# Performance work log

Hardware: AMD Instinct MI355X
Metric: run time of the kernel (lower is better)

## Reference

```python
import jax, jax.numpy as jnp
import numpy as np

N, FIN, F, H = 4096, 128, 64, 8
NEG = -1e10


def setup_inputs() -> dict:
    key = jax.random.key(0)
    ks = jax.random.split(key, 6)
    X = jax.random.normal(ks[0], (N, FIN), dtype=jnp.float32)
    # sparse-ish binary adjacency with self loops, stored dense (as the layer expects)
    A = (jax.random.uniform(ks[1], (N, N)) < 0.05).astype(jnp.int32)
    A = A.at[jnp.arange(N), jnp.arange(N)].set(1)
    W = jax.random.normal(ks[2], (H, FIN, F), dtype=jnp.float32) * (1.0 / np.sqrt(FIN))
    b = jnp.zeros((H, F), dtype=jnp.float32)
    a_self = jax.random.normal(ks[3], (H, F), dtype=jnp.float32) * (1.0 / np.sqrt(F))
    a_neigh = jax.random.normal(ks[4], (H, F), dtype=jnp.float32) * (1.0 / np.sqrt(F))
    return {"X": X, "A": A, "W": W, "b": b, "a_self": a_self, "a_neigh": a_neigh}


def reference(X, A, W, b, a_self, a_neigh):
    # Dropout layers run in inference mode in the original call -> identity.
    feats = jnp.einsum('nf,hfo->hno', X, W)              # [H, N, F]
    s_self = jnp.einsum('hno,ho->hn', feats, a_self)     # [H, N]
    s_neigh = jnp.einsum('hno,ho->hn', feats, a_neigh)   # [H, N]
    scores = s_self[:, :, None] + s_neigh[:, None, :]    # [H, N, N]
    scores = jnp.where(scores > 0, scores, 0.2 * scores)  # LeakyReLU(0.2)
    mask = (1.0 - A.astype(jnp.float32)) * NEG            # [N, N]
    attn = jax.nn.softmax(scores + mask[None], axis=-1)   # [H, N, N]
    out = jnp.einsum('hnm,hmo->hno', attn, feats) + b[:, None, :]
    out = jax.nn.elu(out)                                 # [H, N, F]
    # concat heads -> [N, H*F]
    return jnp.transpose(out, (1, 0, 2)).reshape(N, H * F)
```

## Files before the change

### kernel.cpp

```cpp
#include <hip/hip_runtime.h>
#include <cmath>


#define NN 4096
#define FIN 128
#define FF 64
#define HH 8

typedef _Float16 h2 __attribute__((ext_vector_type(2)));
typedef _Float16 h4 __attribute__((ext_vector_type(4)));
typedef _Float16 h8 __attribute__((ext_vector_type(8)));
typedef float f32x2 __attribute__((ext_vector_type(2)));
typedef float f32x4 __attribute__((ext_vector_type(4)));

union H8 {
  h8 v;
  h2 p[4];
};
union H4 {
  h4 v;
  h2 p[2];
};

static __device__ __forceinline__ float dot2acc(h2 a, float c) {
#if __has_builtin(__builtin_amdgcn_fdot2)
  return __builtin_amdgcn_fdot2(a, (h2){(_Float16)1.f, (_Float16)1.f}, c,
                                false);
#else
  return c + (float)a[0] + (float)a[1];
#endif
}

static __device__ __forceinline__ void gload16(const void* g, void* l) {
  __builtin_amdgcn_global_load_lds(
      (const __attribute__((address_space(1))) unsigned int*)g,
      (__attribute__((address_space(3))) unsigned int*)l, 16, 0, 0);
}

static __device__ __forceinline__ void pack_row(const int* __restrict__ A,
                                                unsigned long long* __restrict__
                                                    bits,
                                                int row, int tid) {
  __shared__ int ldsT[4][4][256];
  const int wave = tid >> 6, lane = tid & 63;
  const int* ar = A + (size_t)row * NN;
  int4 v[4];
#pragma unroll
  for (int it = 0; it < 4; ++it) {
    const int g = wave * 4 + it;
    v[it] = *(const int4*)(ar + g * 256 + lane * 4);
  }
#pragma unroll
  for (int it = 0; it < 4; ++it) *(int4*)&ldsT[wave][it][lane * 4] = v[it];
  unsigned long long* br = bits + ((size_t)row << 6);
#pragma unroll
  for (int it = 0; it < 4; ++it) {
    const int g = wave * 4 + it;
    int w0 = ldsT[wave][it][0 * 64 + lane];
    int w1 = ldsT[wave][it][1 * 64 + lane];
    int w2 = ldsT[wave][it][2 * 64 + lane];
    int w3 = ldsT[wave][it][3 * 64 + lane];
    unsigned long long m0 = __ballot(w0 != 0);
    unsigned long long m1 = __ballot(w1 != 0);
    unsigned long long m2 = __ballot(w2 != 0);
    unsigned long long m3 = __ballot(w3 != 0);
    if (lane == 0) {
      ulonglong2 p0 = {m0, m1}, p1 = {m2, m3};
      *(ulonglong2*)(br + g * 4 + 0) = p0;
      *(ulonglong2*)(br + g * 4 + 2) = p1;
    }
  }
}

__global__ __launch_bounds__(256) void k1_kernel(
    const int* __restrict__ A, const float* __restrict__ W,
    const float* __restrict__ X, unsigned long long* __restrict__ bits,
    _Float16* __restrict__ Wsw, _Float16* __restrict__ Xsw) {
  const int b = blockIdx.x;
  const int tid = threadIdx.x;
  const int wave = tid >> 6, lane = tid & 63;
  if (b < 2) {
    const int h0 = b * 4;
    for (int h = h0; h < h0 + 4; ++h) {
      for (int c = tid; c < 1024; c += 256) {
        int ln = c & 63, nb = (c >> 6) & 3, kt = c >> 8;
        int f = nb * 16 + (ln & 15);
        int k0 = kt * 32 + (ln >> 4) * 8;
        h8 v;
#pragma unroll
        for (int j = 0; j < 8; ++j)
          v[j] = (_Float16)W[((size_t)(h * FIN) + k0 + j) * FF + f];
        *(h8*)(Wsw + ((size_t)(((h * 4 + kt) * 4 + nb) * 64 + ln)) * 8) = v;
      }
    }
  } else if (b < 66) {
    const int tile = (b - 2) * 4 + wave;
    const int l16 = lane & 15, quad = lane >> 4;
    const float* xr = X + (size_t)(tile * 16 + l16) * FIN;
#pragma unroll
    for (int kt = 0; kt < 4; ++kt) {
      int k0 = kt * 32 + quad * 8;
      f32x4 x0 = *(const f32x4*)(xr + k0);
      f32x4 x1 = *(const f32x4*)(xr + k0 + 4);
      h8 v = {(_Float16)x0[0], (_Float16)x0[1], (_Float16)x0[2],
              (_Float16)x0[3], (_Float16)x1[0], (_Float16)x1[1],
              (_Float16)x1[2], (_Float16)x1[3]};
      *(h8*)(Xsw + ((size_t)((tile * 4 + kt) * 64 + lane)) * 8) = v;
    }
  } else {
    pack_row(A, bits, b - 66, tid);
  }
}

__global__ __launch_bounds__(256) void k2_kernel(
    const int* __restrict__ A, unsigned long long* __restrict__ bits,
    const _Float16* __restrict__ Xsw, const _Float16* __restrict__ Wsw,
    const float* __restrict__ a_self, const float* __restrict__ a_neigh,
    _Float16* __restrict__ feats_sw, _Float16* __restrict__ es_h,
    _Float16* __restrict__ esn_h, _Float16* __restrict__ et_h,
    _Float16* __restrict__ etn_h) {
  const int b = blockIdx.x;
  const int tid = threadIdx.x, wave = tid >> 6, lane = tid & 63;
  if (b >= 512) {
    pack_row(A, bits, 2048 + (b - 512), tid);
    return;
  }
  const int rb = b & 63, h = b >> 6;
  const int l16 = lane & 15, quad = lane >> 4;
  const int rt = rb * 4 + wave;
  const int r0 = rt * 16;

  f32x4 acc[4];
#pragma unroll
  for (int nb = 0; nb < 4; ++nb) acc[nb] = (f32x4){0.f, 0.f, 0.f, 0.f};

  const _Float16* xp = Xsw + ((size_t)(rt * 4) * 64 + lane) * 8;
  const _Float16* wp = Wsw + ((size_t)(h * 16) * 64 + lane) * 8;
  h8 Af[4];
#pragma unroll
  for (int kt = 0; kt < 4; ++kt) Af[kt] = *(const h8*)(xp + kt * 512);
#pragma unroll
  for (int kt = 0; kt < 4; ++kt)
#pragma unroll
    for (int nb = 0; nb < 4; ++nb) {
      h8 Bf = *(const h8*)(wp + (kt * 4 + nb) * 512);
      acc[nb] = __builtin_amdgcn_mfma_f32_16x16x32_f16(Af[kt], Bf, acc[nb], 0, 0, 0);
    }

  float as[4], an[4];
#pragma unroll
  for (int nb = 0; nb < 4; ++nb) {
    as[nb] = a_self[h * FF + nb * 16 + l16];
    an[nb] = a_neigh[h * FF + nb * 16 + l16];
  }
#pragma unroll
  for (int r = 0; r < 4; ++r) {
    float ps = acc[0][r] * as[0] + acc[1][r] * as[1] + acc[2][r] * as[2] +
               acc[3][r] * as[3];
    float pn = acc[0][r] * an[0] + acc[1][r] * an[1] + acc[2][r] * an[2] +
               acc[3][r] * an[3];
#pragma unroll
    for (int m = 1; m <= 8; m <<= 1) {
      ps += __shfl_xor(ps, m, 64);
      pn += __shfl_xor(pn, m, 64);
    }
    if (l16 == 0) {
      int node = h * NN + r0 + quad * 4 + r;
      es_h[node] = (_Float16)__expf(ps - 2.0f);
      esn_h[node] = (_Float16)__expf(0.2f * ps - 2.0f);
      et_h[node] = (_Float16)__expf(pn - 2.0f);
      etn_h[node] = (_Float16)__expf(0.2f * pn - 2.0f);
    }
  }

  const int kb = r0 >> 5;
  const int quadA = ((r0 >> 4) & 1) * 2 + (quad >> 1);
  const int jbase = (quad & 1) << 2;
#pragma unroll
  for (int nb = 0; nb < 4; ++nb) {
    h4 v = {(_Float16)acc[nb][0], (_Float16)acc[nb][1], (_Float16)acc[nb][2],
            (_Float16)acc[nb][3]};
    size_t off = ((size_t)((h * 128 + kb) * 4 + nb) << 9) +
                 ((quadA * 16 + l16) << 3) + jbase;
    *(h4*)(feats_sw + off) = v;
  }
}

__global__ __launch_bounds__(512, 4) void attn_kernel(
    const unsigned long long* __restrict__ Abits,
    const _Float16* __restrict__ feats_sw, const _Float16* __restrict__ es_h,
    const _Float16* __restrict__ esn_h, const _Float16* __restrict__ et_h,
    const _Float16* __restrict__ etn_h, const float* __restrict__ bias,
    float* __restrict__ out) {
  const int bid = blockIdx.x;
  const int h = bid & 7, n0 = (bid >> 3) << 6;
  const int tid = threadIdx.x, wave = tid >> 6, lane = tid & 63;
  const int l16 = lane & 15, quad = lane >> 4;
  const int rh = wave & 1, ctw = (wave >> 1) & 1, kfw = wave >> 2;
  const int shTot = (kfw << 5) + (quad << 3);

  __shared__ __align__(16) char smem[3 * 19456];
  __shared__ h4 lutS[16];

  if (tid < 16) {
    h4 m;
#pragma unroll
    for (int j = 0; j < 4; ++j) m[j] = (_Float16)((tid >> j) & 1);
    lutS[tid] = m;
  }
  __syncthreads();

  h2 esp[2], esnp[2];
#pragma unroll
  for (int rt = 0; rt < 2; ++rt) {
    const int myrow = n0 + (rh << 5) + (rt << 4) + l16;
    _Float16 e = es_h[h * NN + myrow];
    _Float16 en = esn_h[h * NN + myrow];
    esp[rt] = (h2){e, e};
    esnp[rt] = (h2){en, en};
  }

  f32x4 acc[2][4], accd[2];
#pragma unroll
  for (int rt = 0; rt < 2; ++rt) {
    accd[rt] = (f32x4){0.f, 0.f, 0.f, 0.f};
#pragma unroll
    for (int nb = 0; nb < 4; ++nb) acc[rt][nb] = (f32x4){0.f, 0.f, 0.f, 0.f};
  }
  const h8 ONES = {(_Float16)1.f, (_Float16)1.f, (_Float16)1.f, (_Float16)1.f,
                   (_Float16)1.f, (_Float16)1.f, (_Float16)1.f, (_Float16)1.f};

  const char* gF = (const char*)feats_sw + ((size_t)h << 19);
  const char* gE = (const char*)et_h + (h << 13);
  const char* gEN = (const char*)etn_h + (h << 13);
  const char* gB = (const char*)Abits + ((size_t)n0 << 9);

#define STAGE(s_, Lp_)                                                         \
  do {                                                                         \
    char* L_ = (char*)(Lp_);                                                   \
    const char* src_ = gF + ((size_t)(s_) << 14) + (wave << 11) + (lane << 4); \
    gload16(src_, L_ + (wave << 11) + (lane << 4));                            \
    gload16(src_ + 1024, L_ + (wave << 11) + 1024 + (lane << 4));              \
    if (wave == 0)                                                             \
      gload16(gE + ((s_) << 8) + (l16 << 4), L_ + 16384 + (lane << 4));        \
    if (wave == 1)                                                             \
      gload16(gEN + ((s_) << 8) + (l16 << 4), L_ + 17408 + (lane << 4));       \
    if (wave == 2)                                                             \
      gload16(gB + ((size_t)lane << 9) + ((s_) << 4), L_ + 18432 + (lane << 4)); \
  } while (0)

#define ITER(s_, SL, NSL, dostage_, last_)                                     \
  {                                                                            \
    __builtin_amdgcn_sched_barrier(0);                                         \
    if (last_) {                                                               \
      asm volatile("s_waitcnt vmcnt(0)" ::: "memory");                         \
    } else if (wave < 3) {                                                     \
      asm volatile("s_waitcnt vmcnt(3)" ::: "memory");                         \
    } else {                                                                   \
      asm volatile("s_waitcnt vmcnt(2)" ::: "memory");                         \
    }                                                                          \
    __builtin_amdgcn_sched_barrier(0);                                         \
    __builtin_amdgcn_s_barrier();                                              \
    if (dostage_) STAGE((s_) + 2, smem + (NSL)*19456);                         \
    const char* L = smem + (SL)*19456;                                         \
    unsigned long long mb0 = *(const unsigned long long*)(                     \
        L + 18432 + (((rh << 5) + l16) << 4) + (ctw << 3));                    \
    unsigned long long mb1 = *(const unsigned long long*)(                     \
        L + 18432 + (((rh << 5) + 16 + l16) << 4) + (ctw << 3));               \
    H8 ET, ETN;                                                                \
    ET.v = *(const h8*)(L + 16384 + (ctw << 7) + (kfw << 6) + (quad << 4));    \
    ETN.v = *(const h8*)(L + 17408 + (ctw << 7) + (kfw << 6) + (quad << 4));   \
    const char* fB = L + (ctw << 13) + (kfw << 12) + (lane << 4);              \
    h8 B0 = *(const h8*)(fB);                                                  \
    h8 B1 = *(const h8*)(fB + 1024);                                           \
    h8 B2 = *(const h8*)(fB + 2048);                                           \
    h8 B3 = *(const h8*)(fB + 3072);                                           \
    _Pragma("unroll") for (int rt = 0; rt < 2; ++rt) {                         \
      const unsigned byt = (unsigned)((rt ? mb1 : mb0) >> shTot) & 0xFFu;      \
      H4 mlo, mhi;                                                             \
      mlo.v = lutS[byt & 15u];                                                 \
      mhi.v = lutS[byt >> 4];                                                  \
      H8 P;                                                                    \
      _Pragma("unroll") for (int p = 0; p < 4; ++p) {                          \
        h2 a_ = esp[rt] * ET.p[p];                                             \
        h2 b_ = esnp[rt] * ETN.p[p];                                           \
        h2 r_ = __builtin_elementwise_max(a_, b_);                             \
        P.p[p] = r_ * (p < 2 ? mlo.p[p] : mhi.p[p - 2]);                       \
      }                                                                        \
      __builtin_amdgcn_s_setprio(1);                                           \
      acc[rt][0] =                                                             \
          __builtin_amdgcn_mfma_f32_16x16x32_f16(P.v, B0, acc[rt][0], 0, 0, 0);\
      acc[rt][1] =                                                             \
          __builtin_amdgcn_mfma_f32_16x16x32_f16(P.v, B1, acc[rt][1], 0, 0, 0);\
      acc[rt][2] =                                                             \
          __builtin_amdgcn_mfma_f32_16x16x32_f16(P.v, B2, acc[rt][2], 0, 0, 0);\
      acc[rt][3] =                                                             \
          __builtin_amdgcn_mfma_f32_16x16x32_f16(P.v, B3, acc[rt][3], 0, 0, 0);\
      accd[rt] =                                                               \
          __builtin_amdgcn_mfma_f32_16x16x32_f16(P.v, ONES, accd[rt], 0, 0, 0);\
      __builtin_amdgcn_s_setprio(0);                                           \
    }                                                                          \
  }

  STAGE(0, smem);
  STAGE(1, smem + 19456);

  for (int sb = 0; sb < 30; sb += 3) {
    ITER(sb + 0, 0, 2, 1, 0);
    ITER(sb + 1, 1, 0, 1, 0);
    ITER(sb + 2, 2, 1, 1, 0);
  }
  ITER(30, 0, 2, 0, 0);
  ITER(31, 1, 0, 0, 1);
#undef ITER
#undef STAGE

  float(*accL)[16][68] = (float(*)[16][68])smem;
  float* denL = (float*)(smem + 8 * 16 * 68 * 4);
  const int erow = tid >> 4;
  const int rh_o = erow >> 4, r16 = erow & 15;
  const int ec0 = (tid & 15) << 2;
#pragma unroll
  for (int rt = 0; rt < 2; ++rt) {
    __syncthreads();
#pragma unroll
    for (int nb = 0; nb < 4; ++nb)
#pragma unroll
      for (int r = 0; r < 4; ++r)
        accL[wave][quad * 4 + r][nb * 16 + l16] = acc[rt][nb][r];
    if (l16 == 0) {
#pragma unroll
      for (int r = 0; r < 4; ++r) denL[wave * 16 + quad * 4 + r] = accd[rt][r];
    }
    __syncthreads();
    f32x4 v = (f32x4){0.f, 0.f, 0.f, 0.f};
    float dn = 0.f;
#pragma unroll
    for (int cw = 0; cw < 4; ++cw) {
      const int w = rh_o + ((cw & 1) << 1) + ((cw >> 1) << 2);
      v += *(const f32x4*)&accL[w][r16][ec0];
      dn += denL[w * 16 + r16];
    }
    float inv = 1.0f / dn;
    const f32x4 bv = *(const f32x4*)(bias + h * FF + ec0);
#pragma unroll
    for (int i = 0; i < 4; ++i) {
      float x = v[i] * inv + bv[i];
      v[i] = x > 0.f ? x : (__expf(x) - 1.0f);
    }
    *(f32x4*)(out + (size_t)(n0 + (rh_o << 5) + (rt << 4) + r16) * (HH * FF) +
              h * FF + ec0) = v;
  }
}

extern "C" void kernel_launch(void* const* d_in, const int* in_sizes, int n_in,
                              void* d_out, int out_size, void* d_ws,
                              size_t ws_size, hipStream_t stream) {
  const float* X = (const float*)d_in[0];
  const int* A = (const int*)d_in[1];
  const float* W = (const float*)d_in[2];
  const float* b = (const float*)d_in[3];
  const float* a_self = (const float*)d_in[4];
  const float* a_neigh = (const float*)d_in[5];
  float* out = (float*)d_out;

  char* ws = (char*)d_ws;
  unsigned long long* Abits = (unsigned long long*)ws;
  _Float16* feats_sw = (_Float16*)(ws + (2u << 20));
  _Float16* es_h = (_Float16*)(ws + (6u << 20));
  _Float16* esn_h = (_Float16*)(ws + (6u << 20) + (64u << 10));
  _Float16* et_h = (_Float16*)(ws + (6u << 20) + (128u << 10));
  _Float16* etn_h = (_Float16*)(ws + (6u << 20) + (192u << 10));
  _Float16* Wsw = (_Float16*)(ws + (6u << 20) + (256u << 10));
  _Float16* Xsw = (_Float16*)(ws + (6u << 20) + (384u << 10));

  k1_kernel<<<66 + 2048, 256, 0, stream>>>(A, W, X, Abits, Wsw, Xsw);
  k2_kernel<<<512 + 2048, 256, 0, stream>>>(A, Abits, Xsw, Wsw, a_self,
                                            a_neigh, feats_sw, es_h, esn_h,
                                            et_h, etn_h);
  attn_kernel<<<512, 512, 0, stream>>>(Abits, feats_sw, es_h, esn_h, et_h,
                                       etn_h, b, out);
}
```

Measured before the change: 141.1 us.

## Prefetch score and mask tiles into registers instead of staging through LDS

The per-stage score vectors and adjacency bitmask words are no longer copied into shared memory by three dedicated waves. Each thread now loads its own slice straight from global memory into registers one stage ahead, using a ping-pong pair of register sets, and the loop is unrolled by six to alternate between them. This shrinks each LDS stage from 19456 to 16384 bytes, which may let more blocks fit per CU, and it removes the uneven wait counts across waves. The cost is more register pressure and duplicated global reads across threads that share the same data, which should mostly hit in cache.

```diff
diff --git a/kernel.cpp b/kernel.cpp
--- a/kernel.cpp
+++ b/kernel.cpp
@@ -21,15 +21,6 @@
   h4 v;
   h2 p[2];
 };
-
-static __device__ __forceinline__ float dot2acc(h2 a, float c) {
-#if __has_builtin(__builtin_amdgcn_fdot2)
-  return __builtin_amdgcn_fdot2(a, (h2){(_Float16)1.f, (_Float16)1.f}, c,
-                                false);
-#else
-  return c + (float)a[0] + (float)a[1];
-#endif
-}
 
 static __device__ __forceinline__ void gload16(const void* g, void* l) {
   __builtin_amdgcn_global_load_lds(
@@ -199,7 +190,7 @@
   const int rh = wave & 1, ctw = (wave >> 1) & 1, kfw = wave >> 2;
   const int shTot = (kfw << 5) + (quad << 3);
 
-  __shared__ __align__(16) char smem[3 * 19456];
+  __shared__ __align__(16) char smem[3 * 16384];
   __shared__ h4 lutS[16];
 
   if (tid < 16) {
@@ -235,55 +226,58 @@
   const char* gEN = (const char*)etn_h + (h << 13);
   const char* gB = (const char*)Abits + ((size_t)n0 << 9);
 
-#define STAGE(s_, Lp_)                                                         \
+  const unsigned eOff = (ctw << 7) + (kfw << 6) + (quad << 4);
+  const unsigned bOff0 = (((rh << 5) + l16) << 9) + (ctw << 3);
+  const unsigned bOff1 = bOff0 + 8192;
+
+  H8 ETa, ETNa, ETb, ETNb;
+  unsigned long long mba0, mba1, mbb0, mbb1;
+
+#define PREF(s_, ET_, ETN_, M0_, M1_)                                          \
   do {                                                                         \
-    char* L_ = (char*)(Lp_);                                                   \
+    ET_.v = *(const h8*)(gE + ((s_) << 8) + eOff);                             \
+    ETN_.v = *(const h8*)(gEN + ((s_) << 8) + eOff);                           \
+    M0_ = *(const unsigned long long*)(gB + bOff0 + ((s_) << 4));              \
+    M1_ = *(const unsigned long long*)(gB + bOff1 + ((s_) << 4));              \
+  } while (0)
+
+#define STAGE(s_, SLOT_)                                                       \
+  do {                                                                         \
+    char* L_ = smem + (SLOT_)*16384;                                           \
     const char* src_ = gF + ((size_t)(s_) << 14) + (wave << 11) + (lane << 4); \
     gload16(src_, L_ + (wave << 11) + (lane << 4));                            \
     gload16(src_ + 1024, L_ + (wave << 11) + 1024 + (lane << 4));              \
-    if (wave == 0)                                                             \
-      gload16(gE + ((s_) << 8) + (l16 << 4), L_ + 16384 + (lane << 4));        \
-    if (wave == 1)                                                             \
-      gload16(gEN + ((s_) << 8) + (l16 << 4), L_ + 17408 + (lane << 4));       \
-    if (wave == 2)                                                             \
-      gload16(gB + ((size_t)lane << 9) + ((s_) << 4), L_ + 18432 + (lane << 4)); \
   } while (0)
 
-#define ITER(s_, SL, NSL, dostage_, last_)                                     \
+#define ITER(s_, SL, NSL, ETu, ETNu, M0u, M1u, ETn, ETNn, M0n, M1n, dopref_,   \
+             dostage_, last_)                                                  \
   {                                                                            \
     __builtin_amdgcn_sched_barrier(0);                                         \
     if (last_) {                                                               \
       asm volatile("s_waitcnt vmcnt(0)" ::: "memory");                         \
-    } else if (wave < 3) {                                                     \
-      asm volatile("s_waitcnt vmcnt(3)" ::: "memory");                         \
     } else {                                                                   \
       asm volatile("s_waitcnt vmcnt(2)" ::: "memory");                         \
     }                                                                          \
     __builtin_amdgcn_sched_barrier(0);                                         \
     __builtin_amdgcn_s_barrier();                                              \
-    if (dostage_) STAGE((s_) + 2, smem + (NSL)*19456);                         \
-    const char* L = smem + (SL)*19456;                                         \
-    unsigned long long mb0 = *(const unsigned long long*)(                     \
-        L + 18432 + (((rh << 5) + l16) << 4) + (ctw << 3));                    \
-    unsigned long long mb1 = *(const unsigned long long*)(                     \
-        L + 18432 + (((rh << 5) + 16 + l16) << 4) + (ctw << 3));               \
-    H8 ET, ETN;                                                                \
-    ET.v = *(const h8*)(L + 16384 + (ctw << 7) + (kfw << 6) + (quad << 4));    \
-    ETN.v = *(const h8*)(L + 17408 + (ctw << 7) + (kfw << 6) + (quad << 4));   \
+    if (dopref_) PREF((s_) + 1, ETn, ETNn, M0n, M1n);                          \
+    if (dostage_) STAGE((s_) + 2, NSL);                                        \
+    __builtin_amdgcn_sched_barrier(0);                                         \
+    const char* L = smem + (SL)*16384;                                         \
     const char* fB = L + (ctw << 13) + (kfw << 12) + (lane << 4);              \
     h8 B0 = *(const h8*)(fB);                                                  \
     h8 B1 = *(const h8*)(fB + 1024);                                           \
     h8 B2 = *(const h8*)(fB + 2048);                                           \
     h8 B3 = *(const h8*)(fB + 3072);                                           \
     _Pragma("unroll") for (int rt = 0; rt < 2; ++rt) {                         \
-      const unsigned byt = (unsigned)((rt ? mb1 : mb0) >> shTot) & 0xFFu;      \
+      const unsigned byt = (unsigned)(((rt ? M1u : M0u) >> shTot)) & 0xFFu;    \
       H4 mlo, mhi;                                                             \
       mlo.v = lutS[byt & 15u];                                                 \
       mhi.v = lutS[byt >> 4];                                                  \
       H8 P;                                                                    \
       _Pragma("unroll") for (int p = 0; p < 4; ++p) {                          \
-        h2 a_ = esp[rt] * ET.p[p];                                             \
-        h2 b_ = esnp[rt] * ETN.p[p];                                           \
+        h2 a_ = esp[rt] * ETu.p[p];                                            \
+        h2 b_ = esnp[rt] * ETNu.p[p];                                          \
         h2 r_ = __builtin_elementwise_max(a_, b_);                             \
         P.p[p] = r_ * (p < 2 ? mlo.p[p] : mhi.p[p - 2]);                       \
       }                                                                        \
@@ -302,18 +296,32 @@
     }                                                                          \
   }
 
-  STAGE(0, smem);
-  STAGE(1, smem + 19456);
-
-  for (int sb = 0; sb < 30; sb += 3) {
-    ITER(sb + 0, 0, 2, 1, 0);
-    ITER(sb + 1, 1, 0, 1, 0);
-    ITER(sb + 2, 2, 1, 1, 0);
-  }
-  ITER(30, 0, 2, 0, 0);
-  ITER(31, 1, 0, 0, 1);
+#define ITER_A(s_, SL, NSL, dopref_, dostage_, last_)                          \
+  ITER(s_, SL, NSL, ETa, ETNa, mba0, mba1, ETb, ETNb, mbb0, mbb1, dopref_,     \
+       dostage_, last_)
+#define ITER_B(s_, SL, NSL, dopref_, dostage_, last_)                          \
+  ITER(s_, SL, NSL, ETb, ETNb, mbb0, mbb1, ETa, ETNa, mba0, mba1, dopref_,     \
+       dostage_, last_)
+
+  PREF(0, ETa, ETNa, mba0, mba1);
+  STAGE(0, 0);
+  STAGE(1, 1);
+
+  for (int sb = 0; sb < 30; sb += 6) {
+    ITER_A(sb + 0, 0, 2, 1, 1, 0);
+    ITER_B(sb + 1, 1, 0, 1, 1, 0);
+    ITER_A(sb + 2, 2, 1, 1, 1, 0);
+    ITER_B(sb + 3, 0, 2, 1, 1, 0);
+    ITER_A(sb + 4, 1, 0, 1, 1, 0);
+    ITER_B(sb + 5, 2, 1, 1, 1, 0);
+  }
+  ITER_A(30, 0, 2, 1, 0, 0);
+  ITER_B(31, 1, 0, 0, 0, 1);
+#undef ITER_A
+#undef ITER_B
 #undef ITER
 #undef STAGE
+#undef PREF
 
   float(*accL)[16][68] = (float(*)[16][68])smem;
   float* denL = (float*)(smem + 8 * 16 * 68 * 4);
```

New measurement: 159.7 us. 13.1% more time.
